# Kernel optimization log

Measured on AMD Instinct MI355X. Metric: run time of the kernel, lower is better.

The kernel has to match this reference:

```python
import jax, jax.numpy as jnp
import numpy as np

B, T, D = 256, 128, 64
H, A, O = 512, 128, 32


def setup_inputs() -> dict:
    key = jax.random.key(0)
    ks = jax.random.split(key, 16)
    u = lambda k, sh, lo, hi: jax.random.uniform(k, sh, jnp.float32, lo, hi)
    return {
        "x_states": jax.random.normal(ks[0], (B, T, D), jnp.float32),
        "x_dts": jax.random.uniform(ks[1], (B, T), jnp.float32) * 0.1,
        # StepwiseAttention params (stored [in, out])
        "Wq": u(ks[2], (D, A), -0.1, 0.1), "bq": u(ks[3], (A,), -0.1, 0.1),
        "Wk": u(ks[4], (H, A), -0.1, 0.1), "bk": u(ks[5], (A,), -0.1, 0.1),
        "Wv": u(ks[6], (H, A), -0.1, 0.1), "bv": u(ks[7], (A,), -0.1, 0.1),
        # LTCAttentionCell params
        "W_gd": u(ks[8], (D + H + A, 2 * H), -0.1, 0.1),
        "b_gd": u(ks[9], (2 * H,), -0.1, 0.1),
        "W_tau": u(ks[10], (H, H), -0.1, 0.1),
        "b_tau": u(ks[11], (H,), -0.1, 0.1),
        "gleak": u(ks[12], (H,), 0.001, 1.0),
        "cm": u(ks[13], (H,), 0.4, 0.6),
        # output head
        "W_fc": u(ks[14], (H, O), -0.1, 0.1),
        "b_fc": u(ks[15], (O,), -0.1, 0.1),
    }


def _forward(x_states, x_dts, Wq, bq, Wk, bk, Wv, bv,
             W_gd, b_gd, W_tau, b_tau, gleak, cm, W_fc, b_fc):
    scale = jnp.sqrt(jnp.asarray(A, jnp.float32))
    leak = jax.nn.softplus(cm) + jax.nn.softplus(gleak)  # [H]

    def dhdt(h, x_t, ctx):
        combined = jnp.concatenate([x_t, h, ctx], axis=1)        # [B, D+H+A]
        gd = combined @ W_gd + b_gd                              # [B, 2H]
        gate, dyn = jnp.split(gd, 2, axis=1)
        tau = jax.nn.softplus(h @ W_tau + b_tau)                 # [B, H]
        num = jax.nn.sigmoid(gate) * jnp.tanh(dyn) - h
        return num / (tau + leak + 1e-6)

    def step(carry, inp):
        h, hist = carry            # h [B,H], hist [B,T,H]
        t, x_t, dt = inp           # t scalar, x_t [B,D], dt [B]
        # stepwise attention over history h_1..h_t
        Q = x_t @ Wq + bq                                        # [B, A]
        K = hist @ Wk + bk                                       # [B, T, A]
        V = hist @ Wv + bv                                       # [B, T, A]
        scores = jnp.einsum('ba,bta->bt', Q, K) / scale          # [B, T]
        valid = jnp.arange(T) < t
        scores = jnp.where(valid[None, :], scores, -1e9)
        w = jax.nn.softmax(scores, axis=-1)
        ctx = jnp.einsum('bt,bta->ba', w, V)
        ctx = jnp.where(t > 0, ctx, jnp.zeros_like(ctx))         # empty history -> 0
        # one RK4 step (torchdiffeq 'rk4' = 3/8-rule variant), step size dt per sample
        dtc = dt[:, None]
        k1 = dhdt(h, x_t, ctx)
        k2 = dhdt(h + dtc * k1 / 3.0, x_t, ctx)
        k3 = dhdt(h + dtc * (k2 - k1 / 3.0), x_t, ctx)
        k4 = dhdt(h + dtc * (k1 - k2 + k3), x_t, ctx)
        h_next = h + dtc * (k1 + 3.0 * k2 + 3.0 * k3 + k4) / 8.0
        hist = jax.lax.dynamic_update_slice(hist, h_next[:, None, :], (0, t, 0))
        return (h_next, hist), None

    h0 = jnp.zeros((B, H), jnp.float32)
    hist0 = jnp.zeros((B, T, H), jnp.float32)
    xs = (jnp.arange(T), jnp.swapaxes(x_states, 0, 1), jnp.swapaxes(x_dts, 0, 1))
    (h_final, _), _ = jax.lax.scan(step, (h0, hist0), xs)
    return h_final @ W_fc + b_fc                                 # [B, O]


def reference(x_states, x_dts, Wq, bq, Wk, bk, Wv, bv,
              W_gd, b_gd, W_tau, b_tau, gleak, cm, W_fc, b_fc):
    return _forward(x_states, x_dts, Wq, bq, Wk, bk, Wv, bv,
                    W_gd, b_gd, W_tau, b_tau, gleak, cm, W_fc, b_fc)
```

## Files before the change

### kernel.cpp

```cpp
#include <hip/hip_runtime.h>
#include <math.h>

#define B_ 256
#define T_ 128
#define D_ 64
#define H_ 512
#define A_ 128
#define O_ 32

typedef __attribute__((ext_vector_type(8))) short short8;
typedef __attribute__((ext_vector_type(8))) unsigned short ushort8;
typedef __attribute__((ext_vector_type(4))) float floatx4;
typedef __attribute__((ext_vector_type(4))) unsigned int uintx4;
typedef unsigned long long ull;

__device__ __forceinline__ float sp_(float x) {
    return fmaxf(x, 0.f) + log1pf(expf(-fabsf(x)));
}
__device__ __forceinline__ float sigm_(float x) {
    return 1.f / (1.f + expf(-x));
}
__device__ __forceinline__ unsigned short f2bf_(float f) {
    unsigned int u = __float_as_uint(f);
    return (unsigned short)((u + 0x7FFFu + ((u >> 16) & 1u)) >> 16);
}
__device__ __forceinline__ float bf2f_(unsigned short u) {
    return __uint_as_float(((unsigned)u) << 16);
}

__device__ __forceinline__ void ld16sc(uintx4& d, const void* p) {
    asm volatile("global_load_dwordx4 %0, %1, off sc0 sc1"
                 : "=v"(d) : "v"(p) : "memory");
}
__device__ __forceinline__ void ld4sc(float& d, const void* p) {
    asm volatile("global_load_dword %0, %1, off sc0 sc1"
                 : "=v"(d) : "v"(p) : "memory");
}
__device__ __forceinline__ void st16sc(unsigned short* p, unsigned v) {
    asm volatile("global_store_short %0, %1, off sc0 sc1"
                 :: "v"(p), "v"(v) : "memory");
}
__device__ __forceinline__ void vmwait4(uintx4& a, uintx4& b, uintx4& c,
                                        uintx4& d) {
    asm volatile("s_waitcnt vmcnt(0)"
                 : "+v"(a), "+v"(b), "+v"(c), "+v"(d)::"memory");
}
__device__ __forceinline__ void vmwait8(uintx4& a, uintx4& b, uintx4& c,
                                        uintx4& d, uintx4& e, uintx4& f,
                                        uintx4& g, uintx4& h) {
    asm volatile("s_waitcnt vmcnt(0)"
                 : "+v"(a), "+v"(b), "+v"(c), "+v"(d), "+v"(e), "+v"(f),
                   "+v"(g), "+v"(h)::"memory");
}
__device__ __forceinline__ void vmwait16f(float& a0, float& a1, float& a2,
                                          float& a3, float& a4, float& a5,
                                          float& a6, float& a7, float& b0,
                                          float& b1, float& b2, float& b3,
                                          float& b4, float& b5, float& b6,
                                          float& b7) {
    asm volatile("s_waitcnt vmcnt(0)"
                 : "+v"(a0), "+v"(a1), "+v"(a2), "+v"(a3), "+v"(a4), "+v"(a5),
                   "+v"(a6), "+v"(a7), "+v"(b0), "+v"(b1), "+v"(b2), "+v"(b3),
                   "+v"(b4), "+v"(b5), "+v"(b6), "+v"(b7)::"memory");
}
__device__ __forceinline__ floatx4 u2f_(uintx4 u) {
    union { uintx4 u; floatx4 f; } c;
    c.u = u;
    return c.f;
}

__device__ __forceinline__ void stf_(float* p, float v) {
    __hip_atomic_store(p, v, __ATOMIC_RELAXED, __HIP_MEMORY_SCOPE_SYSTEM);
}

__global__ void init_kernel(unsigned short* __restrict__ hpack,
                            unsigned* __restrict__ bar) {
    int i = blockIdx.x * 256 + threadIdx.x;
    if (i < B_ * H_) hpack[i] = 0;
    if (i < 8192) bar[i] = 0u;
}

__global__ void pack_w_kernel(const float* __restrict__ W_gd,
                              const float* __restrict__ W_tau,
                              const float* __restrict__ Wk,
                              const float* __restrict__ Wv,
                              unsigned short* __restrict__ Wpack) {
    int gid = blockIdx.x * 256 + threadIdx.x;
    if (gid >= 1114112) return;
    int j = gid & 7;
    int l = (gid >> 3) & 63;
    int kpart = (l >> 4) * 8 + j;
    int npart = l & 15;
    float v;
    if (gid < 786432) {
        int f = gid >> 9;
        int s = f % 3;
        int rem = f / 3;
        int kb = rem & 15, ct = rem >> 4;
        int k = kb * 32 + kpart;
        int c = ct * 16 + npart;
        if (s == 0)      v = W_gd[(size_t)(D_ + k) * 1024 + c];
        else if (s == 1) v = W_gd[(size_t)(D_ + k) * 1024 + 512 + c];
        else             v = W_tau[(size_t)k * 512 + c];
    } else if (gid < 851968) {
        int r = gid - 786432;
        int f = r >> 9;
        int s = f & 1, kb = (f >> 1) & 1, ct = f >> 2;
        int k = kb * 32 + kpart;
        int c = ct * 16 + npart;
        v = W_gd[(size_t)k * 1024 + s * 512 + c];
    } else if (gid < 983040) {
        int r = gid - 851968;
        int f = r >> 9;
        int s = f & 1, kb = (f >> 1) & 3, ct = f >> 3;
        int k = kb * 32 + kpart;
        int c = ct * 16 + npart;
        v = W_gd[(size_t)(D_ + H_ + k) * 1024 + s * 512 + c];
    } else {
        int r = gid - 983040;
        int f = r >> 9;
        int kb = f & 15, c4 = f >> 4;
        int k = kb * 32 + kpart;
        int n = (c4 & 7) * 16 + npart;
        v = (c4 < 8) ? Wk[(size_t)k * A_ + n] : Wv[(size_t)k * A_ + n];
    }
    Wpack[gid] = f2bf_(v);
}

__device__ __forceinline__ void gsyncF(unsigned* flags, int j, unsigned cnt) {
    asm volatile("s_waitcnt vmcnt(0)" ::: "memory");
    __syncthreads();
    if (threadIdx.x == 0)
        __hip_atomic_store(flags + j * 64, cnt, __ATOMIC_RELAXED,
                           __HIP_MEMORY_SCOPE_SYSTEM);
    if (threadIdx.x < 8) {
        while (__hip_atomic_load(flags + threadIdx.x * 64, __ATOMIC_RELAXED,
                                 __HIP_MEMORY_SCOPE_SYSTEM) < cnt) {
            __builtin_amdgcn_s_sleep(1);
        }
    }
    __syncthreads();
}

struct P {
    const float *x, *dts, *Wq, *bq, *bk, *bv, *b_gd, *b_tau, *gleak, *cm,
        *W_fc, *b_fc;
    float *h, *ctx, *out, *Kpart, *Vpart;
    unsigned short* Kh;
    const unsigned short *Wy, *Wx, *Wc, *Wkv;
    unsigned short *hpack, *yapack, *ybpack;
    unsigned* bar;
};

__global__ __launch_bounds__(256, 1) void fused_kernel(P p) {
    const int tid = threadIdx.x;
    const int bid = blockIdx.x;
    const int lane = tid & 63;
    const int wave = tid >> 6;
    const int g = bid & 15;
    const int j = bid >> 4;
    const int ct = j * 4 + wave;
    unsigned* flags = p.bar + g * 512;
    unsigned cnt = 0;

    __shared__ float WqL[D_ * 129];
    __shared__ float xs4[2][D_];
    __shared__ float q4[2][A_];
    __shared__ float sc4[2][T_];
    __shared__ float red[2][2];
    __shared__ __align__(16) unsigned short AsL[32 * 256];
    __shared__ __align__(16) unsigned short As2[2 * 512];
    __shared__ unsigned short VhL[2][A_][136];

    const int quad = lane >> 4;
    const int c = ct * 16 + (lane & 15);
    const float btau = p.b_tau[c];
    const float lk = sp_(p.cm[c]) + sp_(p.gleak[c]) + 1e-6f;
    const float bgd_g = p.b_gd[c];
    const float bgd_d = p.b_gd[512 + c];
    const int aoff = (quad >> 1) * 256 + (lane & 15) * 16 + (quad & 1) * 8;
    const int ybase = g * 8192 + j * 1024 + wave * 256 + (lane & 15);

    const int sub = tid >> 7;
    const int tl = tid & 127;
    const int r = g * 16 + j * 2 + sub;
    const int rrow = r & 15;

    short8 wg[16], wd[16], wt[16];
    short8 wxg[2], wxd[2], wcg[4], wcd[4];
    {
        const short8* Wy8 = (const short8*)p.Wy;
        #pragma unroll
        for (int kb = 0; kb < 16; ++kb) {
            wg[kb] = Wy8[((ct * 16 + kb) * 3 + 0) * 64 + lane];
            wd[kb] = Wy8[((ct * 16 + kb) * 3 + 1) * 64 + lane];
            wt[kb] = Wy8[((ct * 16 + kb) * 3 + 2) * 64 + lane];
        }
        const short8* Wx8 = (const short8*)p.Wx;
        const short8* Wc8 = (const short8*)p.Wc;
        #pragma unroll
        for (int kb = 0; kb < 2; ++kb) {
            wxg[kb] = Wx8[((ct * 2 + kb) * 2 + 0) * 64 + lane];
            wxd[kb] = Wx8[((ct * 2 + kb) * 2 + 1) * 64 + lane];
        }
        #pragma unroll
        for (int kb = 0; kb < 4; ++kb) {
            wcg[kb] = Wc8[((ct * 4 + kb) * 2 + 0) * 64 + lane];
            wcd[kb] = Wc8[((ct * 4 + kb) * 2 + 1) * 64 + lane];
        }
    }

    for (int i = tid; i < D_ * A_; i += 256) {
        int d = i >> 7, a = i & 127;
        WqL[d * 129 + a] = p.Wq[i];
    }

    floatx4 hreg = {0.f, 0.f, 0.f, 0.f};
    floatx4 rk1, rk2, rk3, baseg, based, ycur, dt4;

    const short8* Wkv8 = (const short8*)p.Wkv;

    __syncthreads();

    for (int t = 0; t < T_; ++t) {
        float4 xr[4];
        {
            uintx4 av[4];
            {
                const unsigned short* src = p.hpack + g * 8192;
                #pragma unroll
                for (int i = 0; i < 4; ++i)
                    ld16sc(av[i], src + (size_t)tid * 8 + i * 2048);
            }
            #pragma unroll
            for (int i = 0; i < 4; ++i)
                dt4[i] = p.dts[(g * 16 + quad * 4 + i) * T_ + t];
            {
                const float4* xrow =
                    (const float4*)&p.x[((g * 16 + (lane & 15)) * T_ + t) * D_];
                #pragma unroll
                for (int kb = 0; kb < 2; ++kb) {
                    xr[2 * kb] = xrow[kb * 8 + quad * 2];
                    xr[2 * kb + 1] = xrow[kb * 8 + quad * 2 + 1];
                }
            }
            if (t > 0) {
                float kk[8], vv[8];
                #pragma unroll
                for (int jj = 0; jj < 8; ++jj) {
                    ld4sc(kk[jj],
                          p.Kpart + ((g * 8 + jj) * 16 + rrow) * 128 + tl);
                    ld4sc(vv[jj],
                          p.Vpart + ((g * 8 + jj) * 16 + rrow) * 128 + tl);
                }
                vmwait16f(kk[0], kk[1], kk[2], kk[3], kk[4], kk[5], kk[6],
                          kk[7], vv[0], vv[1], vv[2], vv[3], vv[4], vv[5],
                          vv[6], vv[7]);
                float ks = p.bk[tl], vs = p.bv[tl];
                #pragma unroll
                for (int jj = 0; jj < 8; ++jj) {
                    ks += kk[jj];
                    vs += vv[jj];
                }
                p.Kh[(size_t)(r * T_ + (t - 1)) * A_ + tl] = f2bf_(ks);
                VhL[sub][tl][t - 1] = f2bf_(vs);
            }
            vmwait4(av[0], av[1], av[2], av[3]);
            #pragma unroll
            for (int i = 0; i < 4; ++i)
                ((uintx4*)AsL)[tid + i * 256] = av[i];

            if (tl < 16)
                ((float4*)xs4[sub])[tl] =
                    ((const float4*)&p.x[(r * T_ + t) * D_])[tl];
            __syncthreads();
            float qa = p.bq[tl];
            #pragma unroll 8
            for (int d = 0; d < D_; ++d) qa += xs4[sub][d] * WqL[d * 129 + tl];
            q4[sub][tl] = qa;
            __syncthreads();
            if (t == 0) {
                stf_(p.ctx + r * A_ + tl, 0.f);
            } else {
                const float rscale = 0.08838834764831845f;
                const int grp = tl >> 4, ln = tl & 15;
                float qv[8];
                #pragma unroll
                for (int i = 0; i < 8; ++i) qv[i] = q4[sub][ln * 8 + i];
                for (int s = grp; s < t; s += 8) {
                    ushort8 k8 = *((const ushort8*)(p.Kh +
                                     (size_t)(r * T_ + s) * A_) + ln);
                    float a2 = 0.f;
                    #pragma unroll
                    for (int i = 0; i < 8; ++i) a2 += bf2f_(k8[i]) * qv[i];
                    #pragma unroll
                    for (int off = 8; off > 0; off >>= 1)
                        a2 += __shfl_xor(a2, off, 16);
                    if (ln == 0) sc4[sub][s] = a2 * rscale;
                }
                __syncthreads();
                float mloc = -1e30f;
                for (int s = tl; s < t; s += 128) mloc = fmaxf(mloc, sc4[sub][s]);
                #pragma unroll
                for (int off = 32; off > 0; off >>= 1)
                    mloc = fmaxf(mloc, __shfl_xor(mloc, off, 64));
                if (lane == 0) red[sub][wave & 1] = mloc;
                __syncthreads();
                float m = fmaxf(red[sub][0], red[sub][1]);
                float ssum = 0.f;
                for (int s = tl; s < t; s += 128) {
                    float e = expf(sc4[sub][s] - m);
                    sc4[sub][s] = e;
                    ssum += e;
                }
                #pragma unroll
                for (int off = 32; off > 0; off >>= 1)
                    ssum += __shfl_xor(ssum, off, 64);
                __syncthreads();
                if (lane == 0) red[sub][wave & 1] = ssum;
                __syncthreads();
                float rs = 1.f / (red[sub][0] + red[sub][1]);
                const unsigned short* Vrow = &VhL[sub][tl][0];
                float ca0 = 0.f, ca1 = 0.f;
                int s0 = 0;
                for (; s0 + 16 <= t; s0 += 16) {
                    ushort8 v0 = *(const ushort8*)(Vrow + s0);
                    ushort8 v1 = *(const ushort8*)(Vrow + s0 + 8);
                    #pragma unroll
                    for (int i = 0; i < 8; ++i) {
                        ca0 += sc4[sub][s0 + i] * bf2f_(v0[i]);
                        ca1 += sc4[sub][s0 + 8 + i] * bf2f_(v1[i]);
                    }
                }
                if (s0 + 8 <= t) {
                    ushort8 v0 = *(const ushort8*)(Vrow + s0);
                    #pragma unroll
                    for (int i = 0; i < 8; ++i)
                        ca0 += sc4[sub][s0 + i] * bf2f_(v0[i]);
                    s0 += 8;
                }
                for (; s0 < t; ++s0) ca0 += sc4[sub][s0] * bf2f_(Vrow[s0]);
                stf_(p.ctx + r * A_ + tl, (ca0 + ca1) * rs);
            }
        }
        gsyncF(flags, j, ++cnt);

        {
            const int mrow = lane & 15;
            const float* crow = &p.ctx[(g * 16 + mrow) * A_];
            uintx4 cc[8];
            #pragma unroll
            for (int kb = 0; kb < 4; ++kb) {
                ld16sc(cc[2 * kb], crow + kb * 32 + quad * 8);
                ld16sc(cc[2 * kb + 1], crow + kb * 32 + quad * 8 + 4);
            }

            floatx4 bg = {0.f, 0.f, 0.f, 0.f};
            floatx4 bd = {0.f, 0.f, 0.f, 0.f};
            #pragma unroll
            for (int kb = 0; kb < 2; ++kb) {
                float4 u = xr[2 * kb], v = xr[2 * kb + 1];
                short8 ax;
                ax[0] = (short)f2bf_(u.x); ax[1] = (short)f2bf_(u.y);
                ax[2] = (short)f2bf_(u.z); ax[3] = (short)f2bf_(u.w);
                ax[4] = (short)f2bf_(v.x); ax[5] = (short)f2bf_(v.y);
                ax[6] = (short)f2bf_(v.z); ax[7] = (short)f2bf_(v.w);
                bg = __builtin_amdgcn_mfma_f32_16x16x32_bf16(ax, wxg[kb], bg, 0, 0, 0);
                bd = __builtin_amdgcn_mfma_f32_16x16x32_bf16(ax, wxd[kb], bd, 0, 0, 0);
            }
            floatx4 ag = {0.f, 0.f, 0.f, 0.f};
            floatx4 ad = {0.f, 0.f, 0.f, 0.f};
            floatx4 at = {0.f, 0.f, 0.f, 0.f};
            #pragma unroll
            for (int kb = 0; kb < 16; ++kb) {
                short8 a = *(const short8*)(AsL + kb * 512 + aoff);
                ag = __builtin_amdgcn_mfma_f32_16x16x32_bf16(a, wg[kb], ag, 0, 0, 0);
                ad = __builtin_amdgcn_mfma_f32_16x16x32_bf16(a, wd[kb], ad, 0, 0, 0);
                at = __builtin_amdgcn_mfma_f32_16x16x32_bf16(a, wt[kb], at, 0, 0, 0);
            }
            vmwait8(cc[0], cc[1], cc[2], cc[3], cc[4], cc[5], cc[6], cc[7]);
            #pragma unroll
            for (int kb = 0; kb < 4; ++kb) {
                floatx4 f0 = u2f_(cc[2 * kb]), f1 = u2f_(cc[2 * kb + 1]);
                short8 ac;
                ac[0] = (short)f2bf_(f0[0]); ac[1] = (short)f2bf_(f0[1]);
                ac[2] = (short)f2bf_(f0[2]); ac[3] = (short)f2bf_(f0[3]);
                ac[4] = (short)f2bf_(f1[0]); ac[5] = (short)f2bf_(f1[1]);
                ac[6] = (short)f2bf_(f1[2]); ac[7] = (short)f2bf_(f1[3]);
                bg = __builtin_amdgcn_mfma_f32_16x16x32_bf16(ac, wcg[kb], bg, 0, 0, 0);
                bd = __builtin_amdgcn_mfma_f32_16x16x32_bf16(ac, wcd[kb], bd, 0, 0, 0);
            }
            #pragma unroll
            for (int i = 0; i < 4; ++i) {
                baseg[i] = bg[i] + bgd_g;
                based[i] = bd[i] + bgd_d;
                float gate = ag[i] + baseg[i];
                float dyn = ad[i] + based[i];
                float tau = sp_(at[i] + btau);
                float ki = (sigm_(gate) * tanhf(dyn) - hreg[i]) / (tau + lk);
                rk1[i] = ki;
                float yn = hreg[i] + dt4[i] * ki * (1.f / 3.f);
                ycur[i] = yn;
                st16sc(p.yapack + ybase + (quad * 4 + i) * 16,
                       (unsigned)f2bf_(yn));
            }
        }
        gsyncF(flags, j, ++cnt);

        #pragma unroll 1
        for (int stage = 2; stage <= 4; ++stage) {
            const unsigned short* ysrc =
                (stage == 2) ? p.yapack : (stage == 3) ? p.ybpack : p.yapack;
            unsigned short* ydst =
                (stage == 2) ? p.ybpack : (stage == 3) ? p.yapack : p.hpack;
            {
                const unsigned short* src = ysrc + g * 8192;
                uintx4 av[4];
                #pragma unroll
                for (int i = 0; i < 4; ++i)
                    ld16sc(av[i], src + (size_t)tid * 8 + i * 2048);
                vmwait4(av[0], av[1], av[2], av[3]);
                #pragma unroll
                for (int i = 0; i < 4; ++i)
                    ((uintx4*)AsL)[tid + i * 256] = av[i];
            }
            __syncthreads();
            floatx4 ag = {0.f, 0.f, 0.f, 0.f};
            floatx4 ad = {0.f, 0.f, 0.f, 0.f};
            floatx4 at = {0.f, 0.f, 0.f, 0.f};
            #pragma unroll
            for (int kb = 0; kb < 16; ++kb) {
                short8 a = *(const short8*)(AsL + kb * 512 + aoff);
                ag = __builtin_amdgcn_mfma_f32_16x16x32_bf16(a, wg[kb], ag, 0, 0, 0);
                ad = __builtin_amdgcn_mfma_f32_16x16x32_bf16(a, wd[kb], ad, 0, 0, 0);
                at = __builtin_amdgcn_mfma_f32_16x16x32_bf16(a, wt[kb], at, 0, 0, 0);
            }
            const int lane_p = ((c >> 3) & 3) * 16;
            #pragma unroll
            for (int i = 0; i < 4; ++i) {
                float gate = ag[i] + baseg[i];
                float dyn = ad[i] + based[i];
                float tau = sp_(at[i] + btau);
                float ki = (sigm_(gate) * tanhf(dyn) - ycur[i]) / (tau + lk);
                float yn;
                if (stage == 2) {
                    rk2[i] = ki;
                    yn = hreg[i] + dt4[i] * (ki - rk1[i] * (1.f / 3.f));
                } else if (stage == 3) {
                    rk3[i] = ki;
                    yn = hreg[i] + dt4[i] * (rk1[i] - rk2[i] + ki);
                } else {
                    yn = hreg[i] +
                         dt4[i] * (rk1[i] + 3.f * rk2[i] + 3.f * rk3[i] + ki) * 0.125f;
                    hreg[i] = yn;
                }
                ycur[i] = yn;
                st16sc(ydst + ybase + (quad * 4 + i) * 16,
                       (unsigned)f2bf_(yn));
                if (stage == 4)
                    As2[(wave >> 1) * 512 + (c & 7) +
                        (lane_p + quad * 4 + i) * 8] = f2bf_(yn);
            }
            if (stage == 4) {
                __syncthreads();
                #pragma unroll
                for (int h4 = 0; h4 < 4; ++h4) {
                    const int c4 = wave + h4 * 4;
                    floatx4 acc = {0.f, 0.f, 0.f, 0.f};
                    #pragma unroll
                    for (int kk2 = 0; kk2 < 2; ++kk2) {
                        short8 a = *(const short8*)(As2 + (kk2 * 64 + lane) * 8);
                        acc = __builtin_amdgcn_mfma_f32_16x16x32_bf16(
                            a, Wkv8[(c4 * 16 + (j * 2 + kk2)) * 64 + lane], acc,
                            0, 0, 0);
                    }
                    const int ac = (c4 & 7) * 16 + (lane & 15);
                    float* part = (c4 < 8) ? p.Kpart : p.Vpart;
                    #pragma unroll
                    for (int i = 0; i < 4; ++i)
                        stf_(part + ((g * 8 + j) * 16 + quad * 4 + i) * 128 + ac,
                             acc[i]);
                }
            }
            gsyncF(flags, j, ++cnt);
        }
    }

    #pragma unroll
    for (int i = 0; i < 4; ++i)
        stf_(p.h + (g * 16 + quad * 4 + i) * H_ + c, hreg[i]);
    gsyncF(flags, j, ++cnt);
    {
        const int o = tl & 31, ks = tl >> 5;
        float acc = 0.f;
        const float* hrow = p.h + r * H_ + ks * 128;
        const float* wcol = p.W_fc + ks * 128 * O_ + o;
        #pragma unroll 1
        for (int rd = 0; rd < 4; ++rd) {
            uintx4 hh[8];
            #pragma unroll
            for (int i = 0; i < 8; ++i)
                ld16sc(hh[i], hrow + rd * 32 + i * 4);
            vmwait8(hh[0], hh[1], hh[2], hh[3], hh[4], hh[5], hh[6], hh[7]);
            #pragma unroll
            for (int i = 0; i < 8; ++i) {
                floatx4 f = u2f_(hh[i]);
                #pragma unroll
                for (int e = 0; e < 4; ++e)
                    acc += f[e] * wcol[(rd * 32 + i * 4 + e) * O_];
            }
        }
        sc4[sub][tl] = acc;
        __syncthreads();
        if (ks == 0)
            p.out[r * O_ + o] = acc + sc4[sub][o + 32] + sc4[sub][o + 64] +
                                sc4[sub][o + 96] + p.b_fc[o];
    }
}

extern "C" void kernel_launch(void* const* d_in, const int* in_sizes, int n_in,
                              void* d_out, int out_size, void* d_ws,
                              size_t ws_size, hipStream_t stream) {
    (void)in_sizes; (void)n_in; (void)out_size; (void)ws_size;
    P p;
    p.x = (const float*)d_in[0];
    p.dts = (const float*)d_in[1];
    p.Wq = (const float*)d_in[2];
    p.bq = (const float*)d_in[3];
    const float* Wk = (const float*)d_in[4];
    p.bk = (const float*)d_in[5];
    const float* Wv = (const float*)d_in[6];
    p.bv = (const float*)d_in[7];
    const float* W_gd = (const float*)d_in[8];
    p.b_gd = (const float*)d_in[9];
    const float* W_tau = (const float*)d_in[10];
    p.b_tau = (const float*)d_in[11];
    p.gleak = (const float*)d_in[12];
    p.cm = (const float*)d_in[13];
    p.W_fc = (const float*)d_in[14];
    p.b_fc = (const float*)d_in[15];
    p.out = (float*)d_out;

    float* ws = (float*)d_ws;
    p.h = ws;
    p.ctx = p.h + B_ * H_;
    p.Kpart = p.ctx + B_ * A_;
    p.Vpart = p.Kpart + 262144;
    unsigned short* Wpack = (unsigned short*)(p.Vpart + 262144);
    p.Wy = Wpack;
    p.Wx = Wpack + 786432;
    p.Wc = Wpack + 851968;
    p.Wkv = Wpack + 983040;
    p.hpack = Wpack + 1114112;
    p.yapack = p.hpack + B_ * H_;
    p.ybpack = p.yapack + B_ * H_;
    p.Kh = p.ybpack + B_ * H_;
    p.bar = (unsigned*)(p.Kh + (size_t)B_ * T_ * A_);

    init_kernel<<<512, 256, 0, stream>>>(p.hpack, p.bar);
    pack_w_kernel<<<4352, 256, 0, stream>>>(W_gd, W_tau, Wk, Wv, Wpack);

    fused_kernel<<<dim3(128), dim3(256), 0, stream>>>(p);
}
```

Before: 3.635 ms.

## Compute K/V projections and attention redundantly per block to drop a grid sync

Each block now computes the full K/V projection of the new hidden state for its 16-row group from the gathered hpack tile, instead of splitting it across 8 blocks into partial sums. It also runs attention and ctx for all 16 rows locally, keeping ctx in shared memory. This removes the Kpart/Vpart partial-sum round trip, the global ctx buffer and one group barrier per timestep. Stage outputs are staged in LDS and written as 64-bit stores instead of scattered 16-bit stores. The cost is 8x redundant K/V and attention work per group, plus duplicated writes to the global K/V history.

```diff
diff --git a/kernel.cpp b/kernel.cpp
--- a/kernel.cpp
+++ b/kernel.cpp
@@ -32,12 +32,8 @@
     asm volatile("global_load_dwordx4 %0, %1, off sc0 sc1"
                  : "=v"(d) : "v"(p) : "memory");
 }
-__device__ __forceinline__ void ld4sc(float& d, const void* p) {
-    asm volatile("global_load_dword %0, %1, off sc0 sc1"
-                 : "=v"(d) : "v"(p) : "memory");
-}
-__device__ __forceinline__ void st16sc(unsigned short* p, unsigned v) {
-    asm volatile("global_store_short %0, %1, off sc0 sc1"
+__device__ __forceinline__ void st64sc(ull* p, ull v) {
+    asm volatile("global_store_dwordx2 %0, %1, off sc0 sc1"
                  :: "v"(p), "v"(v) : "memory");
 }
 __device__ __forceinline__ void vmwait4(uintx4& a, uintx4& b, uintx4& c,
@@ -52,23 +48,11 @@
                  : "+v"(a), "+v"(b), "+v"(c), "+v"(d), "+v"(e), "+v"(f),
                    "+v"(g), "+v"(h)::"memory");
 }
-__device__ __forceinline__ void vmwait16f(float& a0, float& a1, float& a2,
-                                          float& a3, float& a4, float& a5,
-                                          float& a6, float& a7, float& b0,
-                                          float& b1, float& b2, float& b3,
-                                          float& b4, float& b5, float& b6,
-                                          float& b7) {
-    asm volatile("s_waitcnt vmcnt(0)"
-                 : "+v"(a0), "+v"(a1), "+v"(a2), "+v"(a3), "+v"(a4), "+v"(a5),
-                   "+v"(a6), "+v"(a7), "+v"(b0), "+v"(b1), "+v"(b2), "+v"(b3),
-                   "+v"(b4), "+v"(b5), "+v"(b6), "+v"(b7)::"memory");
-}
 __device__ __forceinline__ floatx4 u2f_(uintx4 u) {
     union { uintx4 u; floatx4 f; } c;
     c.u = u;
     return c.f;
 }
-
 __device__ __forceinline__ void stf_(float* p, float v) {
     __hip_atomic_store(p, v, __ATOMIC_RELAXED, __HIP_MEMORY_SCOPE_SYSTEM);
 }
@@ -145,8 +129,8 @@
 struct P {
     const float *x, *dts, *Wq, *bq, *bk, *bv, *b_gd, *b_tau, *gleak, *cm,
         *W_fc, *b_fc;
-    float *h, *ctx, *out, *Kpart, *Vpart;
-    unsigned short* Kh;
+    float *h, *out;
+    unsigned short *KhG, *VhG;
     const unsigned short *Wy, *Wx, *Wc, *Wkv;
     unsigned short *hpack, *yapack, *ybpack;
     unsigned* bar;
@@ -164,13 +148,12 @@
     unsigned cnt = 0;
 
     __shared__ float WqL[D_ * 129];
-    __shared__ float xs4[2][D_];
-    __shared__ float q4[2][A_];
-    __shared__ float sc4[2][T_];
-    __shared__ float red[2][2];
+    __shared__ __align__(16) float xsL[16][64];
+    __shared__ float qL[16][A_];
+    __shared__ float scL[16][T_];
+    __shared__ __align__(16) float ctxL[16][132];
     __shared__ __align__(16) unsigned short AsL[32 * 256];
-    __shared__ __align__(16) unsigned short As2[2 * 512];
-    __shared__ unsigned short VhL[2][A_][136];
+    __shared__ __align__(16) unsigned short ypbuf[4 * 256];
 
     const int quad = lane >> 4;
     const int c = ct * 16 + (lane & 15);
@@ -179,12 +162,11 @@
     const float bgd_g = p.b_gd[c];
     const float bgd_d = p.b_gd[512 + c];
     const int aoff = (quad >> 1) * 256 + (lane & 15) * 16 + (quad & 1) * 8;
-    const int ybase = g * 8192 + j * 1024 + wave * 256 + (lane & 15);
+    const int ypw = wave * 256 + (lane & 15);
 
     const int sub = tid >> 7;
     const int tl = tid & 127;
-    const int r = g * 16 + j * 2 + sub;
-    const int rrow = r & 15;
+    const int rfc = g * 16 + j * 2 + sub;
 
     short8 wg[16], wd[16], wt[16];
     short8 wxg[2], wxd[2], wcg[4], wcd[4];
@@ -219,6 +201,9 @@
     floatx4 rk1, rk2, rk3, baseg, based, ycur, dt4;
 
     const short8* Wkv8 = (const short8*)p.Wkv;
+    const int row = tid >> 4;
+    const int k0 = tid & 15;
+    const size_t grow = (size_t)(g * 16 + row);
 
     __syncthreads();
 
@@ -226,12 +211,14 @@
         float4 xr[4];
         {
             uintx4 av[4];
-            {
-                const unsigned short* src = p.hpack + g * 8192;
-                #pragma unroll
-                for (int i = 0; i < 4; ++i)
-                    ld16sc(av[i], src + (size_t)tid * 8 + i * 2048);
-            }
+            const unsigned short* src = p.hpack + g * 8192;
+            #pragma unroll
+            for (int i = 0; i < 4; ++i)
+                ld16sc(av[i], src + (size_t)tid * 8 + i * 2048);
+            if (tid < 64)
+                ((float4*)&xsL[tid >> 2][0])[tid & 3] =
+                    ((const float4*)&p.x[((g * 16 + (tid >> 2)) * T_ + t) *
+                                         D_])[tid & 3];
             #pragma unroll
             for (int i = 0; i < 4; ++i)
                 dt4[i] = p.dts[(g * 16 + quad * 4 + i) * T_ + t];
@@ -244,117 +231,98 @@
                     xr[2 * kb + 1] = xrow[kb * 8 + quad * 2 + 1];
                 }
             }
-            if (t > 0) {
-                float kk[8], vv[8];
-                #pragma unroll
-                for (int jj = 0; jj < 8; ++jj) {
-                    ld4sc(kk[jj],
-                          p.Kpart + ((g * 8 + jj) * 16 + rrow) * 128 + tl);
-                    ld4sc(vv[jj],
-                          p.Vpart + ((g * 8 + jj) * 16 + rrow) * 128 + tl);
-                }
-                vmwait16f(kk[0], kk[1], kk[2], kk[3], kk[4], kk[5], kk[6],
-                          kk[7], vv[0], vv[1], vv[2], vv[3], vv[4], vv[5],
-                          vv[6], vv[7]);
-                float ks = p.bk[tl], vs = p.bv[tl];
-                #pragma unroll
-                for (int jj = 0; jj < 8; ++jj) {
-                    ks += kk[jj];
-                    vs += vv[jj];
-                }
-                p.Kh[(size_t)(r * T_ + (t - 1)) * A_ + tl] = f2bf_(ks);
-                VhL[sub][tl][t - 1] = f2bf_(vs);
-            }
             vmwait4(av[0], av[1], av[2], av[3]);
             #pragma unroll
             for (int i = 0; i < 4; ++i)
                 ((uintx4*)AsL)[tid + i * 256] = av[i];
-
-            if (tl < 16)
-                ((float4*)xs4[sub])[tl] =
-                    ((const float4*)&p.x[(r * T_ + t) * D_])[tl];
-            __syncthreads();
-            float qa = p.bq[tl];
-            #pragma unroll 8
-            for (int d = 0; d < D_; ++d) qa += xs4[sub][d] * WqL[d * 129 + tl];
-            q4[sub][tl] = qa;
-            __syncthreads();
-            if (t == 0) {
-                stf_(p.ctx + r * A_ + tl, 0.f);
-            } else {
-                const float rscale = 0.08838834764831845f;
-                const int grp = tl >> 4, ln = tl & 15;
-                float qv[8];
-                #pragma unroll
-                for (int i = 0; i < 8; ++i) qv[i] = q4[sub][ln * 8 + i];
-                for (int s = grp; s < t; s += 8) {
-                    ushort8 k8 = *((const ushort8*)(p.Kh +
-                                     (size_t)(r * T_ + s) * A_) + ln);
-                    float a2 = 0.f;
-                    #pragma unroll
-                    for (int i = 0; i < 8; ++i) a2 += bf2f_(k8[i]) * qv[i];
-                    #pragma unroll
-                    for (int off = 8; off > 0; off >>= 1)
-                        a2 += __shfl_xor(a2, off, 16);
-                    if (ln == 0) sc4[sub][s] = a2 * rscale;
+        }
+        __syncthreads();
+
+        if (t > 0) {
+            #pragma unroll
+            for (int h4 = 0; h4 < 4; ++h4) {
+                const int c4 = wave + h4 * 4;
+                floatx4 acc = {0.f, 0.f, 0.f, 0.f};
+                #pragma unroll
+                for (int kb = 0; kb < 16; ++kb) {
+                    short8 a = *(const short8*)(AsL + kb * 512 + aoff);
+                    acc = __builtin_amdgcn_mfma_f32_16x16x32_bf16(
+                        a, Wkv8[(c4 * 16 + kb) * 64 + lane], acc, 0, 0, 0);
                 }
-                __syncthreads();
-                float mloc = -1e30f;
-                for (int s = tl; s < t; s += 128) mloc = fmaxf(mloc, sc4[sub][s]);
-                #pragma unroll
-                for (int off = 32; off > 0; off >>= 1)
-                    mloc = fmaxf(mloc, __shfl_xor(mloc, off, 64));
-                if (lane == 0) red[sub][wave & 1] = mloc;
-                __syncthreads();
-                float m = fmaxf(red[sub][0], red[sub][1]);
-                float ssum = 0.f;
-                for (int s = tl; s < t; s += 128) {
-                    float e = expf(sc4[sub][s] - m);
-                    sc4[sub][s] = e;
-                    ssum += e;
+                const int ac = (c4 & 7) * 16 + (lane & 15);
+                unsigned short* dst = (c4 < 8) ? p.KhG : p.VhG;
+                const float bias = ((c4 < 8) ? p.bk : p.bv)[ac];
+                #pragma unroll
+                for (int i = 0; i < 4; ++i) {
+                    size_t rr = (size_t)(g * 16 + quad * 4 + i);
+                    dst[(rr * T_ + (t - 1)) * A_ + ac] = f2bf_(acc[i] + bias);
                 }
-                #pragma unroll
-                for (int off = 32; off > 0; off >>= 1)
-                    ssum += __shfl_xor(ssum, off, 64);
-                __syncthreads();
-                if (lane == 0) red[sub][wave & 1] = ssum;
-                __syncthreads();
-                float rs = 1.f / (red[sub][0] + red[sub][1]);
-                const unsigned short* Vrow = &VhL[sub][tl][0];
-                float ca0 = 0.f, ca1 = 0.f;
-                int s0 = 0;
-                for (; s0 + 16 <= t; s0 += 16) {
-                    ushort8 v0 = *(const ushort8*)(Vrow + s0);
-                    ushort8 v1 = *(const ushort8*)(Vrow + s0 + 8);
-                    #pragma unroll
-                    for (int i = 0; i < 8; ++i) {
-                        ca0 += sc4[sub][s0 + i] * bf2f_(v0[i]);
-                        ca1 += sc4[sub][s0 + 8 + i] * bf2f_(v1[i]);
-                    }
-                }
-                if (s0 + 8 <= t) {
-                    ushort8 v0 = *(const ushort8*)(Vrow + s0);
+            }
+        }
+        {
+            float qa[8];
+            #pragma unroll
+            for (int n = 0; n < 8; ++n) qa[n] = p.bq[k0 * 8 + n];
+            for (int d = 0; d < D_; ++d) {
+                float xv = xsL[row][d];
+                #pragma unroll
+                for (int n = 0; n < 8; ++n)
+                    qa[n] += xv * WqL[d * 129 + k0 * 8 + n];
+            }
+            #pragma unroll
+            for (int n = 0; n < 8; ++n) qL[row][k0 * 8 + n] = qa[n];
+        }
+        asm volatile("s_waitcnt vmcnt(0)" ::: "memory");
+        __syncthreads();
+
+        if (t > 0) {
+            const float rscale = 0.08838834764831845f;
+            for (int s = k0; s < t; s += 16) {
+                const ushort8* K8 =
+                    (const ushort8*)&p.KhG[(grow * T_ + s) * A_];
+                float a2 = 0.f;
+                #pragma unroll
+                for (int w8 = 0; w8 < 16; ++w8) {
+                    ushort8 k8 = K8[w8];
                     #pragma unroll
                     for (int i = 0; i < 8; ++i)
-                        ca0 += sc4[sub][s0 + i] * bf2f_(v0[i]);
-                    s0 += 8;
+                        a2 += bf2f_(k8[i]) * qL[row][w8 * 8 + i];
                 }
-                for (; s0 < t; ++s0) ca0 += sc4[sub][s0] * bf2f_(Vrow[s0]);
-                stf_(p.ctx + r * A_ + tl, (ca0 + ca1) * rs);
-            }
-        }
-        gsyncF(flags, j, ++cnt);
+                scL[row][s] = a2 * rscale;
+            }
+            float m = -1e30f;
+            for (int s = k0; s < t; s += 16) m = fmaxf(m, scL[row][s]);
+            #pragma unroll
+            for (int off = 8; off > 0; off >>= 1)
+                m = fmaxf(m, __shfl_xor(m, off, 16));
+            float ssum = 0.f;
+            for (int s = k0; s < t; s += 16) {
+                float e = expf(scL[row][s] - m);
+                scL[row][s] = e;
+                ssum += e;
+            }
+            #pragma unroll
+            for (int off = 8; off > 0; off >>= 1)
+                ssum += __shfl_xor(ssum, off, 16);
+            float rs = 1.f / ssum;
+            __syncthreads();
+            float ca[8] = {0.f, 0.f, 0.f, 0.f, 0.f, 0.f, 0.f, 0.f};
+            for (int s = 0; s < t; ++s) {
+                float w = scL[row][s];
+                ushort8 v8 = *(const ushort8*)&p.VhG[(grow * T_ + s) * A_ +
+                                                     k0 * 8];
+                #pragma unroll
+                for (int i = 0; i < 8; ++i) ca[i] += w * bf2f_(v8[i]);
+            }
+            #pragma unroll
+            for (int i = 0; i < 8; ++i) ctxL[row][k0 * 8 + i] = ca[i] * rs;
+        } else {
+            #pragma unroll
+            for (int i = 0; i < 8; ++i) ctxL[row][k0 * 8 + i] = 0.f;
+        }
+        __syncthreads();
 
         {
-            const int mrow = lane & 15;
-            const float* crow = &p.ctx[(g * 16 + mrow) * A_];
-            uintx4 cc[8];
-            #pragma unroll
-            for (int kb = 0; kb < 4; ++kb) {
-                ld16sc(cc[2 * kb], crow + kb * 32 + quad * 8);
-                ld16sc(cc[2 * kb + 1], crow + kb * 32 + quad * 8 + 4);
-            }
-
             floatx4 bg = {0.f, 0.f, 0.f, 0.f};
             floatx4 bd = {0.f, 0.f, 0.f, 0.f};
             #pragma unroll
@@ -368,6 +336,19 @@
                 bg = __builtin_amdgcn_mfma_f32_16x16x32_bf16(ax, wxg[kb], bg, 0, 0, 0);
                 bd = __builtin_amdgcn_mfma_f32_16x16x32_bf16(ax, wxd[kb], bd, 0, 0, 0);
             }
+            const int mrow = lane & 15;
+            #pragma unroll
+            for (int kb = 0; kb < 4; ++kb) {
+                float4 f0 = *(const float4*)&ctxL[mrow][kb * 32 + quad * 8];
+                float4 f1 = *(const float4*)&ctxL[mrow][kb * 32 + quad * 8 + 4];
+                short8 ac;
+                ac[0] = (short)f2bf_(f0.x); ac[1] = (short)f2bf_(f0.y);
+                ac[2] = (short)f2bf_(f0.z); ac[3] = (short)f2bf_(f0.w);
+                ac[4] = (short)f2bf_(f1.x); ac[5] = (short)f2bf_(f1.y);
+                ac[6] = (short)f2bf_(f1.z); ac[7] = (short)f2bf_(f1.w);
+                bg = __builtin_amdgcn_mfma_f32_16x16x32_bf16(ac, wcg[kb], bg, 0, 0, 0);
+                bd = __builtin_amdgcn_mfma_f32_16x16x32_bf16(ac, wcd[kb], bd, 0, 0, 0);
+            }
             floatx4 ag = {0.f, 0.f, 0.f, 0.f};
             floatx4 ad = {0.f, 0.f, 0.f, 0.f};
             floatx4 at = {0.f, 0.f, 0.f, 0.f};
@@ -377,18 +358,6 @@
                 ag = __builtin_amdgcn_mfma_f32_16x16x32_bf16(a, wg[kb], ag, 0, 0, 0);
                 ad = __builtin_amdgcn_mfma_f32_16x16x32_bf16(a, wd[kb], ad, 0, 0, 0);
                 at = __builtin_amdgcn_mfma_f32_16x16x32_bf16(a, wt[kb], at, 0, 0, 0);
-            }
-            vmwait8(cc[0], cc[1], cc[2], cc[3], cc[4], cc[5], cc[6], cc[7]);
-            #pragma unroll
-            for (int kb = 0; kb < 4; ++kb) {
-                floatx4 f0 = u2f_(cc[2 * kb]), f1 = u2f_(cc[2 * kb + 1]);
-                short8 ac;
-                ac[0] = (short)f2bf_(f0[0]); ac[1] = (short)f2bf_(f0[1]);
-                ac[2] = (short)f2bf_(f0[2]); ac[3] = (short)f2bf_(f0[3]);
-                ac[4] = (short)f2bf_(f1[0]); ac[5] = (short)f2bf_(f1[1]);
-                ac[6] = (short)f2bf_(f1[2]); ac[7] = (short)f2bf_(f1[3]);
-                bg = __builtin_amdgcn_mfma_f32_16x16x32_bf16(ac, wcg[kb], bg, 0, 0, 0);
-                bd = __builtin_amdgcn_mfma_f32_16x16x32_bf16(ac, wcd[kb], bd, 0, 0, 0);
             }
             #pragma unroll
             for (int i = 0; i < 4; ++i) {
@@ -401,9 +370,11 @@
                 rk1[i] = ki;
                 float yn = hreg[i] + dt4[i] * ki * (1.f / 3.f);
                 ycur[i] = yn;
-                st16sc(p.yapack + ybase + (quad * 4 + i) * 16,
-                       (unsigned)f2bf_(yn));
-            }
+                ypbuf[ypw + (quad * 4 + i) * 16] = f2bf_(yn);
+            }
+            __syncthreads();
+            st64sc((ull*)p.yapack + g * 2048 + j * 256 + tid,
+                   ((const ull*)ypbuf)[tid]);
         }
         gsyncF(flags, j, ++cnt);
 
@@ -435,7 +406,6 @@
                 ad = __builtin_amdgcn_mfma_f32_16x16x32_bf16(a, wd[kb], ad, 0, 0, 0);
                 at = __builtin_amdgcn_mfma_f32_16x16x32_bf16(a, wt[kb], at, 0, 0, 0);
             }
-            const int lane_p = ((c >> 3) & 3) * 16;
             #pragma unroll
             for (int i = 0; i < 4; ++i) {
                 float gate = ag[i] + baseg[i];
@@ -455,33 +425,11 @@
                     hreg[i] = yn;
                 }
                 ycur[i] = yn;
-                st16sc(ydst + ybase + (quad * 4 + i) * 16,
-                       (unsigned)f2bf_(yn));
-                if (stage == 4)
-                    As2[(wave >> 1) * 512 + (c & 7) +
-                        (lane_p + quad * 4 + i) * 8] = f2bf_(yn);
-            }
-            if (stage == 4) {
-                __syncthreads();
-                #pragma unroll
-                for (int h4 = 0; h4 < 4; ++h4) {
-                    const int c4 = wave + h4 * 4;
-                    floatx4 acc = {0.f, 0.f, 0.f, 0.f};
-                    #pragma unroll
-                    for (int kk2 = 0; kk2 < 2; ++kk2) {
-                        short8 a = *(const short8*)(As2 + (kk2 * 64 + lane) * 8);
-                        acc = __builtin_amdgcn_mfma_f32_16x16x32_bf16(
-                            a, Wkv8[(c4 * 16 + (j * 2 + kk2)) * 64 + lane], acc,
-                            0, 0, 0);
-                    }
-                    const int ac = (c4 & 7) * 16 + (lane & 15);
-                    float* part = (c4 < 8) ? p.Kpart : p.Vpart;
-                    #pragma unroll
-                    for (int i = 0; i < 4; ++i)
-                        stf_(part + ((g * 8 + j) * 16 + quad * 4 + i) * 128 + ac,
-                             acc[i]);
-                }
-            }
+                ypbuf[ypw + (quad * 4 + i) * 16] = f2bf_(yn);
+            }
+            __syncthreads();
+            st64sc((ull*)ydst + g * 2048 + j * 256 + tid,
+                   ((const ull*)ypbuf)[tid]);
             gsyncF(flags, j, ++cnt);
         }
     }
@@ -491,9 +439,10 @@
         stf_(p.h + (g * 16 + quad * 4 + i) * H_ + c, hreg[i]);
     gsyncF(flags, j, ++cnt);
     {
+        float* fcred = (float*)scL;
         const int o = tl & 31, ks = tl >> 5;
         float acc = 0.f;
-        const float* hrow = p.h + r * H_ + ks * 128;
+        const float* hrow = p.h + rfc * H_ + ks * 128;
         const float* wcol = p.W_fc + ks * 128 * O_ + o;
         #pragma unroll 1
         for (int rd = 0; rd < 4; ++rd) {
@@ -510,11 +459,12 @@
                     acc += f[e] * wcol[(rd * 32 + i * 4 + e) * O_];
             }
         }
-        sc4[sub][tl] = acc;
+        fcred[tid] = acc;
         __syncthreads();
         if (ks == 0)
-            p.out[r * O_ + o] = acc + sc4[sub][o + 32] + sc4[sub][o + 64] +
-                                sc4[sub][o + 96] + p.b_fc[o];
+            p.out[rfc * O_ + o] = acc + fcred[sub * 128 + o + 32] +
+                                  fcred[sub * 128 + o + 64] +
+                                  fcred[sub * 128 + o + 96] + p.b_fc[o];
     }
 }
 
@@ -543,10 +493,7 @@
 
     float* ws = (float*)d_ws;
     p.h = ws;
-    p.ctx = p.h + B_ * H_;
-    p.Kpart = p.ctx + B_ * A_;
-    p.Vpart = p.Kpart + 262144;
-    unsigned short* Wpack = (unsigned short*)(p.Vpart + 262144);
+    unsigned short* Wpack = (unsigned short*)(p.h + B_ * H_);
     p.Wy = Wpack;
     p.Wx = Wpack + 786432;
     p.Wc = Wpack + 851968;
@@ -554,8 +501,9 @@
     p.hpack = Wpack + 1114112;
     p.yapack = p.hpack + B_ * H_;
     p.ybpack = p.yapack + B_ * H_;
-    p.Kh = p.ybpack + B_ * H_;
-    p.bar = (unsigned*)(p.Kh + (size_t)B_ * T_ * A_);
+    p.KhG = p.ybpack + B_ * H_;
+    p.VhG = p.KhG + (size_t)B_ * T_ * A_;
+    p.bar = (unsigned*)(p.VhG + (size_t)B_ * T_ * A_);
 
     init_kernel<<<512, 256, 0, stream>>>(p.hpack, p.bar);
     pack_w_kernel<<<4352, 256, 0, stream>>>(W_gd, W_tau, Wk, Wv, Wpack);
```

New measurement: 7.364 ms. 2.03x slower.
